# Kernel optimization log

Hardware: AMD Instinct MI355X
Metric: run time of the kernel (lower is better)

The kernel has to match this reference:

```python
import jax, jax.numpy as jnp
import numpy as np

D = 768
NH = 12
HD = D // NH
T = 8
HW = 14
B = 16
BT = B * T
NTOK = 1 + HW * HW  # 197
DH = int(D * 0.25)  # adapter hidden = 192
SCALE = 0.5


def _ln(x, g, b, eps=1e-5):
    # fp32 LayerNorm (matches LayerNorm subclass casting to fp32)
    xf = x.astype(jnp.float32)
    m = xf.mean(-1, keepdims=True)
    v = ((xf - m) ** 2).mean(-1, keepdims=True)
    return (((xf - m) / jnp.sqrt(v + eps)) * g + b).astype(x.dtype)


def _adapter(x, w1, b1, w2, b2, skip):
    h = jax.nn.gelu(x @ w1.T + b1, approximate=False)
    h = h @ w2.T + b2
    return x + h if skip else h


def _attention(xq, ykv, in_w, in_b, out_w, out_b):
    # xq: [Tx, N, D], ykv: [Ty, N, D]
    q = xq @ in_w[:D].T + in_b[:D]
    k = ykv @ in_w[D:2 * D].T + in_b[D:2 * D]
    v = ykv @ in_w[2 * D:].T + in_b[2 * D:]
    Tx, N, _ = q.shape
    Ty = k.shape[0]
    q = q.reshape(Tx, N, NH, HD).transpose(1, 2, 0, 3)  # [N,h,Tx,hd]
    k = k.reshape(Ty, N, NH, HD).transpose(1, 2, 0, 3)
    v = v.reshape(Ty, N, NH, HD).transpose(1, 2, 0, 3)
    aff = jnp.einsum('nhqd,nhkd->nhqk', q, k) / jnp.asarray(np.sqrt(HD), q.dtype)
    aff = jax.nn.softmax(aff, axis=-1)
    out = jnp.einsum('nhqk,nhkd->nhqd', aff, v)
    out = out.transpose(2, 0, 1, 3).reshape(Tx, N, D)
    return out @ out_w.T + out_b


_SHIFTS = (((0, 0), -4), ((0, 1), 1), ((1, 0), -1), ((0, 2), 2),
           ((2, 0), -2), ((1, 2), 3), ((2, 1), -3), ((2, 2), 4))


def _patch_shift(x):
    # x: [B, T, H, W, C]; roll along time on strided spatial grids
    out = x
    for (i, j), s in _SHIFTS:
        out = out.at[:, :, i::3, j::3, :].set(jnp.roll(x[:, :, i::3, j::3, :], s, axis=1))
    return out


def _forward(x, in_w, in_b, out_w, out_b, ln1_g, ln1_b, ln2_g, ln2_b,
             fc_w, fc_b, proj_w, proj_b,
             t1_w, t1_b, t2_w, t2_b,
             s1_w, s1_b, s2_w, s2_b,
             m1_w, m1_b, m2_w, m2_b):
    n, bt, d = x.shape
    b = bt // T
    # temporal attention on class token
    cls = x[:1]  # [1, bt, d]
    xt = cls.reshape(1, b, T, d).transpose(2, 1, 0, 3).reshape(T, b, d)
    xtn = _ln(xt, ln1_g, ln1_b)
    xt = _attention(xtn, xtn, in_w, in_b, out_w, out_b)
    xt = _adapter(xt, t1_w, t1_b, t2_w, t2_b, skip=False)
    xt = xt.reshape(T, b, 1, d).transpose(2, 1, 0, 3).reshape(1, bt, d)
    x = jnp.concatenate([x[:1], xt, x[1:]], axis=0)  # [n+1, bt, d]
    # spatial attention with patch shift (extra shifted K/V tokens)
    xln = _ln(x, ln1_g, ln1_b)
    tmp = xln[2:]  # [HW*HW, bt, d]
    tmp = tmp.reshape(HW, HW, b, T, d).transpose(2, 3, 0, 1, 4)  # b t h w c
    tmp = _patch_shift(tmp)
    tmp = tmp.transpose(2, 3, 0, 1, 4).reshape(HW * HW, bt, d)
    kv = jnp.concatenate([xln, tmp], axis=0)  # [2n+... , bt, d]
    attn_out = _attention(xln, kv, in_w, in_b, out_w, out_b)
    x = x + _adapter(attn_out, s1_w, s1_b, s2_w, s2_b, skip=True)
    # drop temporal token
    x = jnp.concatenate([x[:1], x[2:]], axis=0)
    # MLP + scaled MLP adapter
    xn = _ln(x, ln2_g, ln2_b)
    h = xn @ fc_w.T + fc_b
    h = h * jax.nn.sigmoid(1.702 * h)  # QuickGELU
    mlp = h @ proj_w.T + proj_b
    x = x + mlp + SCALE * _adapter(xn, m1_w, m1_b, m2_w, m2_b, skip=False)
    return x


def setup_inputs() -> dict:
    key = jax.random.key(0)
    ks = jax.random.split(key, 16)
    s = 0.02
    inp = {
        'x': jax.random.normal(ks[0], (NTOK, BT, D), jnp.float32),
        'in_w': jax.random.normal(ks[1], (3 * D, D), jnp.float32) * s,
        'in_b': jnp.zeros((3 * D,), jnp.float32),
        'out_w': jax.random.normal(ks[2], (D, D), jnp.float32) * s,
        'out_b': jnp.zeros((D,), jnp.float32),
        'ln1_g': jnp.ones((D,), jnp.float32),
        'ln1_b': jnp.zeros((D,), jnp.float32),
        'ln2_g': jnp.ones((D,), jnp.float32),
        'ln2_b': jnp.zeros((D,), jnp.float32),
        'fc_w': jax.random.normal(ks[3], (4 * D, D), jnp.float32) * s,
        'fc_b': jnp.zeros((4 * D,), jnp.float32),
        'proj_w': jax.random.normal(ks[4], (D, 4 * D), jnp.float32) * s,
        'proj_b': jnp.zeros((D,), jnp.float32),
        't1_w': jax.random.normal(ks[5], (DH, D), jnp.float32) * s,
        't1_b': jnp.zeros((DH,), jnp.float32),
        't2_w': jax.random.normal(ks[6], (D, DH), jnp.float32) * s,
        't2_b': jnp.zeros((D,), jnp.float32),
        's1_w': jax.random.normal(ks[7], (DH, D), jnp.float32) * s,
        's1_b': jnp.zeros((DH,), jnp.float32),
        's2_w': jax.random.normal(ks[8], (D, DH), jnp.float32) * s,
        's2_b': jnp.zeros((D,), jnp.float32),
        'm1_w': jax.random.normal(ks[9], (DH, D), jnp.float32) * s,
        'm1_b': jnp.zeros((DH,), jnp.float32),
        'm2_w': jax.random.normal(ks[10], (D, DH), jnp.float32) * s,
        'm2_b': jnp.zeros((D,), jnp.float32),
    }
    return inp


def reference(x, in_w, in_b, out_w, out_b, ln1_g, ln1_b, ln2_g, ln2_b,
              fc_w, fc_b, proj_w, proj_b,
              t1_w, t1_b, t2_w, t2_b,
              s1_w, s1_b, s2_w, s2_b,
              m1_w, m1_b, m2_w, m2_b):
    return _forward(x, in_w, in_b, out_w, out_b, ln1_g, ln1_b, ln2_g, ln2_b,
                    fc_w, fc_b, proj_w, proj_b,
                    t1_w, t1_b, t2_w, t2_b,
                    s1_w, s1_b, s2_w, s2_b,
                    m1_w, m1_b, m2_w, m2_b)
```

## Files before the change

kernel.cpp:

```cpp
#include <hip/hip_runtime.h>
#include <hip/hip_bf16.h>


#define DEV static __device__ __forceinline__

constexpr int D     = 768;
constexpr int TT    = 8;
constexpr int BT    = 128;
constexpr int NTOK  = 197;
constexpr int NTOK2 = 198;
constexpr int NKV   = 394;
constexpr int NKVP  = 448;
constexpr int NQP   = 224;
constexpr int NSZ   = 64;
constexpr int MQ    = NTOK2 * NSZ;
constexpr int MKV   = NKV   * NSZ;
constexpr int KCAT  = 3264;

constexpr int R2 = NTOK2 * BT;
constexpr int R3 = NTOK  * BT;

constexpr size_t O_WB  = 0;
constexpr size_t O_XLN = 3981312;
constexpr size_t O_AO  = O_XLN + 9732096;
constexpr size_t O_QT  = O_AO  + 9732096;
constexpr size_t O_KT  = O_QT  + 5505024;
constexpr size_t O_VT  = O_KT  + 11010048;
constexpr size_t O_SM  = O_VT  + 11010048;
constexpr size_t O_XT   = O_SM;
constexpr size_t O_XTN  = O_XT  + 98304;
constexpr size_t O_QKVT = O_XTN + 49152;
constexpr size_t O_AT   = O_QKVT+ 294912;
constexpr size_t O_ATP  = O_AT  + 49152;
constexpr size_t O_TH   = O_ATP + 49152;
constexpr size_t O_XT2  = O_TH  + 12288;
constexpr size_t O_MQ   = O_XT2 + 98304;
constexpr size_t O_MKV  = O_MQ  + 12672;
constexpr size_t O_CB   = O_MKV + 25216;

constexpr size_t WB_INW = 0;
constexpr size_t WB_OUTW= 1769472;
constexpr size_t WB_FCW = 2359296;
constexpr size_t WB_T1W = 7077888;
constexpr size_t WB_T2W = 7225344;
constexpr size_t WB_S1W = 7372800;
constexpr size_t WB_S2W = 7520256;
constexpr size_t WB_M1W = 7667712;

typedef __attribute__((ext_vector_type(8))) short bf16x8;
typedef __attribute__((ext_vector_type(4))) float f32x4;
#define MFMA16 __builtin_amdgcn_mfma_f32_16x16x32_bf16

DEV float bf2f(unsigned short u) { return __uint_as_float(((unsigned)u) << 16); }
DEV unsigned short f2bf(float f) {
    unsigned u = __float_as_uint(f);
    u += 0x7fffu + ((u >> 16) & 1u);
    return (unsigned short)(u >> 16);
}

DEV void gll16(const unsigned short* g, unsigned short* l) {
    __builtin_amdgcn_global_load_lds(
        (const __attribute__((address_space(1))) void*)g,
        (__attribute__((address_space(3))) void*)l, 16, 0, 0);
}

__global__ __launch_bounds__(256) void convert_k(const float* __restrict__ src,
                                                 unsigned short* __restrict__ dst, int n)
{
    int i = blockIdx.x * 256 + threadIdx.x;
    if (i < n) dst[i] = f2bf(src[i]);
}

__global__ __launch_bounds__(256) void convert2d_k(const float* __restrict__ src,
    int rows, int cols, int sld, unsigned short* __restrict__ dst, int dld, float scale)
{
    int i = blockIdx.x * 256 + threadIdx.x;
    if (i >= rows * cols) return;
    int r = i / cols, c = i % cols;
    dst[(size_t)r * dld + c] = f2bf(src[(size_t)r * sld + c] * scale);
}

__global__ __launch_bounds__(256) void combine_bias_k(const float* __restrict__ a,
    const float* __restrict__ b, float* __restrict__ cb)
{
    int i = blockIdx.x * 256 + threadIdx.x;
    if (i < 768) cb[i] = a[i] + 0.5f * b[i];
}

template<int EPI, int OMODE>
__global__ __launch_bounds__(256) void gemm_mfma_k(
    const unsigned short* __restrict__ A, const int* __restrict__ rowmap,
    const unsigned short* __restrict__ Wb, int wlda,
    const float* __restrict__ bias, float bscale,
    float* __restrict__ Yf, unsigned short* __restrict__ Yb,
    int N, int K, int ldy, const float* __restrict__ Xf)
{
    __shared__ unsigned short Als[128][32];
    __shared__ unsigned short Wls[64][32];
    const int tid = threadIdx.x;
    const int n0 = blockIdx.x * 64, m0 = blockIdx.y * 128;
    const int w = tid >> 6, l = tid & 63;

    int ga0 = m0 + w * 32 + (l >> 2);
    int ga1 = ga0 + 16;
    const int gw = n0 + w * 16 + (l >> 2);
    if (rowmap) { ga0 = rowmap[ga0]; ga1 = rowmap[ga1]; }
    const unsigned short* Ap0 = A + (size_t)ga0 * K + (l & 3) * 8;
    const unsigned short* Ap1 = A + (size_t)ga1 * K + (l & 3) * 8;
    const unsigned short* Wp  = Wb + (size_t)gw * wlda + (l & 3) * 8;
    unsigned short* lA0 = &Als[w * 32 + (l >> 2)][(l & 3) * 8];
    unsigned short* lA1 = &Als[w * 32 + 16 + (l >> 2)][(l & 3) * 8];
    unsigned short* lW  = &Wls[w * 16 + (l >> 2)][(l & 3) * 8];

    f32x4 acc[2][4];
    #pragma unroll
    for (int r = 0; r < 2; ++r)
        #pragma unroll
        for (int c = 0; c < 4; ++c)
            acc[r][c] = (f32x4){0.f, 0.f, 0.f, 0.f};

    for (int k0 = 0; k0 < K; k0 += 32) {
        __syncthreads();
        gll16(Ap0 + k0, lA0);
        gll16(Ap1 + k0, lA1);
        gll16(Wp  + k0, lW);
        __syncthreads();

        bf16x8 af[2], bfr[4];
        #pragma unroll
        for (int r = 0; r < 2; ++r)
            af[r] = *(const bf16x8*)&Als[w * 32 + r * 16 + (l & 15)][(l >> 4) * 8];
        #pragma unroll
        for (int c = 0; c < 4; ++c)
            bfr[c] = *(const bf16x8*)&Wls[c * 16 + (l & 15)][(l >> 4) * 8];
        #pragma unroll
        for (int r = 0; r < 2; ++r)
            #pragma unroll
            for (int c = 0; c < 4; ++c)
                acc[r][c] = MFMA16(af[r], bfr[c], acc[r][c], 0, 0, 0);
    }

    #pragma unroll
    for (int r = 0; r < 2; ++r) {
        #pragma unroll
        for (int c = 0; c < 4; ++c) {
            const int colg = n0 + c * 16 + (l & 15);
            const float bv = bscale * bias[colg];
            #pragma unroll
            for (int i = 0; i < 4; ++i) {
                const int rowg = m0 + w * 32 + r * 16 + ((l >> 4) << 2) + i;
                float v = acc[r][c][i] + bv;
                if (EPI == 1) v = 0.5f * v * (1.f + erff(v * 0.70710678118654752f));
                else if (EPI == 2) v = v / (1.f + __expf(-1.702f * v));
                if (OMODE == 0) {
                    Yf[(size_t)rowg * ldy + colg] = v;
                } else if (OMODE == 1) {
                    Yb[(size_t)rowg * ldy + colg] = f2bf(v);
                } else if (OMODE == 3) {
                    int j = rowg >> 6, bbl = rowg & 63, h = colg >> 6, d = colg & 63;
                    Yb[(((size_t)bbl * 12 + h) * NKVP + j) * 64 + d] = f2bf(v);
                } else if (OMODE == 5) {
                    int j = rowg >> 6, bbl = rowg & 63, h = colg >> 6, d = colg & 63;
                    Yb[(((size_t)bbl * 12 + h) * NQP + j) * 64 + d] = f2bf(v * 0.125f);
                } else if (OMODE == 6) {
                    Yf[(size_t)rowg * ldy + colg] += v;
                } else if (OMODE == 8) {
                    int tok2 = rowg >> 7, bb2 = rowg & 127;
                    if (tok2 != 1) {
                        int otok = tok2 ? tok2 - 1 : 0;
                        size_t oi = ((size_t)(otok * BT + bb2)) * ldy + colg;
                        Yf[oi] = Xf[oi] + bf2f(Yb[(size_t)rowg * ldy + colg]) + v;
                    }
                }
            }
        }
    }
}

template<typename TO>
__global__ __launch_bounds__(256) void ln_k(
    const float* __restrict__ in, TO* __restrict__ out,
    const float* __restrict__ g, const float* __restrict__ b, int rows)
{
    int w = (int)((blockIdx.x * 256 + threadIdx.x) >> 6);
    int lane = threadIdx.x & 63;
    if (w >= rows) return;
    const float* x = in + (size_t)w * D;
    float v[12];
    float s = 0.f;
    #pragma unroll
    for (int i = 0; i < 12; ++i) { v[i] = x[lane + 64 * i]; s += v[i]; }
    #pragma unroll
    for (int m = 32; m; m >>= 1) s += __shfl_xor(s, m);
    float mean = s * (1.f / 768.f);
    float s2 = 0.f;
    #pragma unroll
    for (int i = 0; i < 12; ++i) { float d0 = v[i] - mean; s2 += d0 * d0; }
    #pragma unroll
    for (int m = 32; m; m >>= 1) s2 += __shfl_xor(s2, m);
    float rstd = rsqrtf(s2 * (1.f / 768.f) + 1e-5f);
    TO* o = out + (size_t)w * D;
    #pragma unroll
    for (int i = 0; i < 12; ++i) {
        int c = lane + 64 * i;
        float y = (v[i] - mean) * rstd * g[c] + b[c];
        if constexpr (sizeof(TO) == 2) o[c] = f2bf(y); else o[c] = y;
    }
}

__global__ __launch_bounds__(256) void ln_gather_k(
    const float* __restrict__ x, const float* __restrict__ xt2,
    unsigned short* __restrict__ out,
    const float* __restrict__ g, const float* __restrict__ b)
{
    int w = (int)((blockIdx.x * 256 + threadIdx.x) >> 6);
    int lane = threadIdx.x & 63;
    if (w >= R2) return;
    int tok = w >> 7, bb = w & 127;
    const float* src;
    if (tok == 0)      src = x + (size_t)bb * D;
    else if (tok == 1) src = xt2 + (size_t)((bb & 7) * 16 + (bb >> 3)) * D;
    else               src = x + ((size_t)(tok - 1) * BT + bb) * D;
    float v[12];
    float s = 0.f;
    #pragma unroll
    for (int i = 0; i < 12; ++i) { v[i] = src[lane + 64 * i]; s += v[i]; }
    #pragma unroll
    for (int m = 32; m; m >>= 1) s += __shfl_xor(s, m);
    float mean = s * (1.f / 768.f);
    float s2 = 0.f;
    #pragma unroll
    for (int i = 0; i < 12; ++i) { float d0 = v[i] - mean; s2 += d0 * d0; }
    #pragma unroll
    for (int m = 32; m; m >>= 1) s2 += __shfl_xor(s2, m);
    float rstd = rsqrtf(s2 * (1.f / 768.f) + 1e-5f);
    unsigned short* o = out + (size_t)w * D;
    #pragma unroll
    for (int i = 0; i < 12; ++i) {
        int c = lane + 64 * i;
        o[c] = f2bf((v[i] - mean) * rstd * g[c] + b[c]);
    }
}

__global__ __launch_bounds__(256) void gather_cls_k(const float* __restrict__ x, float* __restrict__ xt)
{
    int idx = blockIdx.x * 256 + threadIdx.x;
    if (idx >= 128 * 768) return;
    int row = idx / 768, c = idx % 768;
    int t = row >> 4, bsel = row & 15;
    xt[idx] = x[(size_t)(bsel * TT + t) * D + c];
}

__global__ __launch_bounds__(64) void attn_temporal_k(
    const float* __restrict__ QKVt, unsigned short* __restrict__ Ot)
{
    int n = blockIdx.x, h = blockIdx.y;
    int lane = threadIdx.x;
    __shared__ float qs[8][64], ks[8][64], vs[8][64];
    __shared__ float ps[8][9];
    {
        int t = lane >> 3, f8 = lane & 7;
        size_t rb = ((size_t)(t * 16 + n)) * 2304 + h * 64 + f8 * 8;
        *(float4*)&qs[t][f8 * 8]     = *(const float4*)&QKVt[rb];
        *(float4*)&qs[t][f8 * 8 + 4] = *(const float4*)&QKVt[rb + 4];
        *(float4*)&ks[t][f8 * 8]     = *(const float4*)&QKVt[rb + 768];
        *(float4*)&ks[t][f8 * 8 + 4] = *(const float4*)&QKVt[rb + 772];
        *(float4*)&vs[t][f8 * 8]     = *(const float4*)&QKVt[rb + 1536];
        *(float4*)&vs[t][f8 * 8 + 4] = *(const float4*)&QKVt[rb + 1540];
    }
    __syncthreads();
    int qt = lane >> 3, kt = lane & 7;
    float s = 0.f;
    #pragma unroll
    for (int d0 = 0; d0 < 64; ++d0) s += qs[qt][d0] * ks[kt][d0];
    s *= 0.125f;
    float mx = s;
    #pragma unroll
    for (int m = 4; m; m >>= 1) mx = fmaxf(mx, __shfl_xor(mx, m));
    float p = __expf(s - mx), sum = p;
    #pragma unroll
    for (int m = 4; m; m >>= 1) sum += __shfl_xor(sum, m);
    ps[qt][kt] = p / sum;
    __syncthreads();
    int dg = lane & 7;
    float o[8] = {};
    #pragma unroll
    for (int k2 = 0; k2 < 8; ++k2) {
        float pp = ps[qt][k2];
        #pragma unroll
        for (int dd = 0; dd < 8; ++dd) o[dd] += pp * vs[k2][dg * 8 + dd];
    }
    unsigned short* op = &Ot[((size_t)(qt * 16 + n)) * D + h * 64 + dg * 8];
    #pragma unroll
    for (int dd = 0; dd < 8; ++dd) op[dd] = f2bf(o[dd]);
}

__global__ __launch_bounds__(256) void build_maps_k(int* __restrict__ mq,
                                                    int* __restrict__ mkv, int nbase)
{
    int idx = blockIdx.x * 256 + threadIdx.x;
    if (idx < MQ) {
        int j = idx >> 6, bbl = idx & 63;
        mq[idx] = j * BT + nbase + bbl;
    }
    int k = idx - MQ;
    if (k >= 0 && k < MKV) {
        int j = k >> 6, bb = nbase + (k & 63);
        int src;
        if (j < NTOK2) src = j * BT + bb;
        else {
            const int stab[9] = {-4, 1, 2, -1, 0, 3, -2, -3, 4};
            int p = j - NTOK2, r = p / 14, c = p % 14;
            int s = stab[(r % 3) * 3 + (c % 3)];
            int b = bb >> 3, t = bb & 7;
            int t2 = (t - s) & 7;
            src = (2 + p) * BT + b * TT + t2;
        }
        mkv[k] = src;
    }
}

__global__ __launch_bounds__(256) void attn_mfma_k(
    const unsigned short* __restrict__ Qt, const unsigned short* __restrict__ Kt,
    const unsigned short* __restrict__ Vt, unsigned short* __restrict__ AO, int nbase)
{
    const int qt0 = blockIdx.x * 32;
    const int h = blockIdx.y, nloc = blockIdx.z;
    const int tid = threadIdx.x, w = tid >> 6, l = tid & 63;
    __shared__ float Sls[32][68];
    __shared__ unsigned short Pls[32][72];
    __shared__ unsigned short Vls[64][72];
    __shared__ float mrun[32], lrun[32], alphals[32];

    const size_t baseQ = ((size_t)(nloc * 12 + h)) * NQP * 64;
    const size_t baseK = ((size_t)(nloc * 12 + h)) * NKVP * 64;

    bf16x8 qf[2][2];
    #pragma unroll
    for (int qb = 0; qb < 2; ++qb)
        #pragma unroll
        for (int ds = 0; ds < 2; ++ds)
            qf[qb][ds] = *(const bf16x8*)&Qt[baseQ + (size_t)(qt0 + qb * 16 + (l & 15)) * 64 + ds * 32 + (l >> 4) * 8];

    if (tid < 32) { mrun[tid] = -3e30f; lrun[tid] = 0.f; }
    f32x4 of[2];
    of[0] = (f32x4){0.f, 0.f, 0.f, 0.f};
    of[1] = (f32x4){0.f, 0.f, 0.f, 0.f};
    __syncthreads();

    for (int kv0 = 0; kv0 < NKV; kv0 += 64) {
        #pragma unroll
        for (int p = 0; p < 2; ++p) {
            int idx = tid + p * 256;
            int j = idx >> 3, seg = idx & 7;
            uint4 vv = *(const uint4*)&Vt[baseK + (size_t)(kv0 + j) * 64 + seg * 8];
            const unsigned short* pv = (const unsigned short*)&vv;
            #pragma unroll
            for (int e = 0; e < 8; ++e) Vls[seg * 8 + e][j] = pv[e];
        }
        f32x4 sa[2];
        sa[0] = (f32x4){0.f, 0.f, 0.f, 0.f};
        sa[1] = (f32x4){0.f, 0.f, 0.f, 0.f};
        #pragma unroll
        for (int ds = 0; ds < 2; ++ds) {
            bf16x8 kf = *(const bf16x8*)&Kt[baseK + (size_t)(kv0 + w * 16 + (l & 15)) * 64 + ds * 32 + (l >> 4) * 8];
            #pragma unroll
            for (int qb = 0; qb < 2; ++qb)
                sa[qb] = MFMA16(qf[qb][ds], kf, sa[qb], 0, 0, 0);
        }
        #pragma unroll
        for (int qb = 0; qb < 2; ++qb)
            #pragma unroll
            for (int i = 0; i < 4; ++i)
                Sls[qb * 16 + ((l >> 4) << 2) + i][w * 16 + (l & 15)] = sa[qb][i];
        __syncthreads();

        {
            int row = tid >> 3, cg = tid & 7;
            float sv[8], pv[8];
            float mx = -3e30f;
            #pragma unroll
            for (int j = 0; j < 8; ++j) {
                int c = cg * 8 + j;
                float s = (kv0 + c < NKV) ? Sls[row][c] : -3e30f;
                sv[j] = s; mx = fmaxf(mx, s);
            }
            mx = fmaxf(mx, __shfl_xor(mx, 1));
            mx = fmaxf(mx, __shfl_xor(mx, 2));
            mx = fmaxf(mx, __shfl_xor(mx, 4));
            float mold = mrun[row];
            float mnew = fmaxf(mold, mx);
            float ps = 0.f;
            #pragma unroll
            for (int j = 0; j < 8; ++j) { float p = __expf(sv[j] - mnew); pv[j] = p; ps += p; }
            ps += __shfl_xor(ps, 1);
            ps += __shfl_xor(ps, 2);
            ps += __shfl_xor(ps, 4);
            if (cg == 0) {
                float al = __expf(mold - mnew);
                alphals[row] = al;
                mrun[row] = mnew;
                lrun[row] = lrun[row] * al + ps;
            }
            #pragma unroll
            for (int j = 0; j < 8; ++j) Pls[row][cg * 8 + j] = f2bf(pv[j]);
        }
        __syncthreads();

        #pragma unroll
        for (int qb = 0; qb < 2; ++qb) {
            #pragma unroll
            for (int i = 0; i < 4; ++i)
                of[qb][i] *= alphals[qb * 16 + ((l >> 4) << 2) + i];
        }
        #pragma unroll
        for (int ks = 0; ks < 2; ++ks) {
            bf16x8 vf = *(const bf16x8*)&Vls[w * 16 + (l & 15)][ks * 32 + (l >> 4) * 8];
            #pragma unroll
            for (int qb = 0; qb < 2; ++qb) {
                bf16x8 pf = *(const bf16x8*)&Pls[qb * 16 + (l & 15)][ks * 32 + (l >> 4) * 8];
                of[qb] = MFMA16(pf, vf, of[qb], 0, 0, 0);
            }
        }
        __syncthreads();
    }

    #pragma unroll
    for (int qb = 0; qb < 2; ++qb) {
        #pragma unroll
        for (int i = 0; i < 4; ++i) {
            int qrow = qb * 16 + ((l >> 4) << 2) + i;
            int q = qt0 + qrow;
            if (q < NTOK2) {
                float inv = 1.f / lrun[qrow];
                AO[((size_t)q * BT + nbase + nloc) * D + h * 64 + w * 16 + (l & 15)] = f2bf(of[qb][i] * inv);
            }
        }
    }
}

extern "C" void kernel_launch(void* const* d_in, const int* in_sizes, int n_in,
                              void* d_out, int out_size, void* d_ws, size_t ws_size,
                              hipStream_t stream)
{
    const float* x    = (const float*)d_in[0];
    const float* in_w = (const float*)d_in[1];
    const float* in_b = (const float*)d_in[2];
    const float* outw = (const float*)d_in[3];
    const float* outb = (const float*)d_in[4];
    const float* ln1g = (const float*)d_in[5];
    const float* ln1b = (const float*)d_in[6];
    const float* ln2g = (const float*)d_in[7];
    const float* ln2b = (const float*)d_in[8];
    const float* fcw  = (const float*)d_in[9];
    const float* fcb  = (const float*)d_in[10];
    const float* pjw  = (const float*)d_in[11];
    const float* pjb  = (const float*)d_in[12];
    const float* t1w  = (const float*)d_in[13];
    const float* t1b  = (const float*)d_in[14];
    const float* t2w  = (const float*)d_in[15];
    const float* t2b  = (const float*)d_in[16];
    const float* s1w  = (const float*)d_in[17];
    const float* s1b  = (const float*)d_in[18];
    const float* s2w  = (const float*)d_in[19];
    const float* s2b  = (const float*)d_in[20];
    const float* m1w  = (const float*)d_in[21];
    const float* m1b  = (const float*)d_in[22];
    const float* m2w  = (const float*)d_in[23];
    const float* m2b  = (const float*)d_in[24];

    float* ws  = (float*)d_ws;
    float* out = (float*)d_out;

    unsigned short* WB = (unsigned short*)(ws + O_WB);
    unsigned short* w_in  = WB + WB_INW;
    unsigned short* w_out = WB + WB_OUTW;
    unsigned short* w_fc  = WB + WB_FCW;
    unsigned short* w_t1  = WB + WB_T1W;
    unsigned short* w_t2  = WB + WB_T2W;
    unsigned short* w_s1  = WB + WB_S1W;
    unsigned short* w_s2  = WB + WB_S2W;
    unsigned short* w_m1  = WB + WB_M1W;

    unsigned short* xln  = (unsigned short*)(ws + O_XLN);
    unsigned short* AO   = (unsigned short*)(ws + O_AO);
    unsigned short* Qt   = (unsigned short*)(ws + O_QT);
    unsigned short* Kt   = (unsigned short*)(ws + O_KT);
    unsigned short* Vt   = (unsigned short*)(ws + O_VT);
    unsigned short* ao2b = xln;
    unsigned short* xn   = AO;
    unsigned short* h192 = Qt;
    unsigned short* pjcat= (unsigned short*)(ws + O_QT + 2433024);
    unsigned short* catb = Kt;

    float* xt            = ws + O_XT;
    unsigned short* xtn  = (unsigned short*)(ws + O_XTN);
    float* qkvt          = ws + O_QKVT;
    unsigned short* at   = (unsigned short*)(ws + O_AT);
    unsigned short* atp  = (unsigned short*)(ws + O_ATP);
    unsigned short* th   = (unsigned short*)(ws + O_TH);
    float* xt2           = ws + O_XT2;
    int*   mapq          = (int*)(ws + O_MQ);
    int*   mapkv         = (int*)(ws + O_MKV);
    float* cb            = ws + O_CB;

    auto conv = [&](const float* s, unsigned short* dst, int n) {
        convert_k<<<(n + 255) / 256, 256, 0, stream>>>(s, dst, n);
    };
    conv(in_w, w_in, 2304 * 768);
    conv(outw, w_out, 768 * 768);
    conv(fcw,  w_fc,  3072 * 768);
    conv(t1w,  w_t1,  192 * 768);
    conv(t2w,  w_t2,  768 * 192);
    conv(s1w,  w_s1,  192 * 768);
    conv(s2w,  w_s2,  768 * 192);
    conv(m1w,  w_m1,  192 * 768);
    combine_bias_k<<<3, 256, 0, stream>>>(pjb, m2b, cb);

    gather_cls_k<<<384, 256, 0, stream>>>(x, xt);
    ln_k<unsigned short><<<32, 256, 0, stream>>>(xt, xtn, ln1g, ln1b, 128);
    gemm_mfma_k<0,0><<<dim3(36,1), 256, 0, stream>>>(xtn, nullptr, w_in, 768, in_b, 1.f, qkvt, nullptr, 2304, 768, 2304, nullptr);
    attn_temporal_k<<<dim3(16,12), 64, 0, stream>>>(qkvt, at);
    gemm_mfma_k<0,1><<<dim3(12,1), 256, 0, stream>>>(at,  nullptr, w_out, 768, outb, 1.f, nullptr, atp, 768, 768, 768, nullptr);
    gemm_mfma_k<1,1><<<dim3(3,1),  256, 0, stream>>>(atp, nullptr, w_t1,  768, t1b, 1.f, nullptr, th,  192, 768, 192, nullptr);
    gemm_mfma_k<0,0><<<dim3(12,1), 256, 0, stream>>>(th,  nullptr, w_t2,  192, t2b, 1.f, xt2, nullptr, 768, 192, 768, nullptr);

    ln_gather_k<<<6336, 256, 0, stream>>>(x, xt2, xln, ln1g, ln1b);

    for (int c = 0; c < 2; ++c) {
        const int nbase = c * NSZ;
        build_maps_k<<<148, 256, 0, stream>>>(mapq, mapkv, nbase);
        gemm_mfma_k<0,5><<<dim3(12,99),  256, 0, stream>>>(xln, mapq,  w_in,              768, in_b,        1.f, nullptr, Qt, 768, 768, 768, nullptr);
        gemm_mfma_k<0,3><<<dim3(12,197), 256, 0, stream>>>(xln, mapkv, w_in + 768 * 768,  768, in_b + 768,  1.f, nullptr, Kt, 768, 768, 768, nullptr);
        gemm_mfma_k<0,3><<<dim3(12,197), 256, 0, stream>>>(xln, mapkv, w_in + 1536 * 768, 768, in_b + 1536, 1.f, nullptr, Vt, 768, 768, 768, nullptr);
        attn_mfma_k<<<dim3(7,12,64), 256, 0, stream>>>(Qt, Kt, Vt, AO, nbase);
    }

    convert2d_k<<<9216, 256, 0, stream>>>(pjw, 768, 3072, 3072, pjcat, KCAT, 1.f);
    convert2d_k<<<576,  256, 0, stream>>>(m2w, 768, 192, 192, pjcat + 3072, KCAT, 0.5f);

    gemm_mfma_k<0,1><<<dim3(12,198), 256, 0, stream>>>(AO,   nullptr, w_out, 768, outb, 1.f, nullptr, ao2b, 768, 768, 768, nullptr);
    gemm_mfma_k<1,1><<<dim3(3,198),  256, 0, stream>>>(ao2b, nullptr, w_s1,  768, s1b,  1.f, nullptr, h192, 192, 768, 192, nullptr);
    gemm_mfma_k<0,8><<<dim3(12,198), 256, 0, stream>>>(h192, nullptr, w_s2,  192, s2b,  1.f, out, ao2b, 768, 192, 768, x);

    ln_k<unsigned short><<<6304, 256, 0, stream>>>(out, xn, ln2g, ln2b, R3);
    const int nbm[4] = {49, 49, 49, 50};
    int moff = 0;
    for (int mc = 0; mc < 4; ++mc) {
        const int nb = nbm[mc];
        gemm_mfma_k<2,1><<<dim3(48,nb), 256, 0, stream>>>(xn + (size_t)moff * 768, nullptr, w_fc, 768, fcb, 1.f, nullptr, catb, 3072, 768, KCAT, nullptr);
        gemm_mfma_k<1,1><<<dim3(3,nb),  256, 0, stream>>>(xn + (size_t)moff * 768, nullptr, w_m1, 768, m1b, 1.f, nullptr, catb + 3072, 192, 768, KCAT, nullptr);
        gemm_mfma_k<0,6><<<dim3(12,nb), 256, 0, stream>>>(catb, nullptr, pjcat, KCAT, cb, 1.f, out + (size_t)moff * 768, nullptr, 768, KCAT, 768, nullptr);
        moff += nb * 128;
    }
}
```

Baseline: 1.670 ms.

## Add 128x128 MFMA GEMM tile and loop attention over query tiles per block

Adds a 128x128-tile GEMM kernel (each wave computes a 64x64 sub-tile) and uses it for every GEMM whose N is a multiple of 128. The 64-wide kernel is kept for the N=192 adapter layers. The goal is higher arithmetic intensity and fewer redundant A-tile loads. The attention kernel now loops over all query tiles inside one block per (head, batch), instead of one block per query tile. This cuts block count and may improve K/V cache reuse, but it lowers parallelism and reloads K/V per query tile serially.

```diff
diff --git a/kernel.cpp b/kernel.cpp
--- a/kernel.cpp
+++ b/kernel.cpp
@@ -88,12 +88,111 @@
 }
 
 template<int EPI, int OMODE>
-__global__ __launch_bounds__(256) void gemm_mfma_k(
+DEV void epi_store(float v0, int rowg, int colg, const float* bias, float bscale,
+                   float* Yf, unsigned short* Yb, int ldy, const float* Xf)
+{
+    float v = v0 + bscale * bias[colg];
+    if (EPI == 1) v = 0.5f * v * (1.f + erff(v * 0.70710678118654752f));
+    else if (EPI == 2) v = v / (1.f + __expf(-1.702f * v));
+    if (OMODE == 0) {
+        Yf[(size_t)rowg * ldy + colg] = v;
+    } else if (OMODE == 1) {
+        Yb[(size_t)rowg * ldy + colg] = f2bf(v);
+    } else if (OMODE == 3) {
+        int j = rowg >> 6, bbl = rowg & 63, h = colg >> 6, d = colg & 63;
+        Yb[(((size_t)bbl * 12 + h) * NKVP + j) * 64 + d] = f2bf(v);
+    } else if (OMODE == 5) {
+        int j = rowg >> 6, bbl = rowg & 63, h = colg >> 6, d = colg & 63;
+        Yb[(((size_t)bbl * 12 + h) * NQP + j) * 64 + d] = f2bf(v * 0.125f);
+    } else if (OMODE == 6) {
+        Yf[(size_t)rowg * ldy + colg] += v;
+    } else if (OMODE == 8) {
+        int tok2 = rowg >> 7, bb2 = rowg & 127;
+        if (tok2 != 1) {
+            int otok = tok2 ? tok2 - 1 : 0;
+            size_t oi = ((size_t)(otok * BT + bb2)) * ldy + colg;
+            Yf[oi] = Xf[oi] + bf2f(Yb[(size_t)rowg * ldy + colg]) + v;
+        }
+    }
+}
+
+template<int EPI, int OMODE>
+__global__ __launch_bounds__(256) void gemm128_k(
     const unsigned short* __restrict__ A, const int* __restrict__ rowmap,
     const unsigned short* __restrict__ Wb, int wlda,
     const float* __restrict__ bias, float bscale,
     float* __restrict__ Yf, unsigned short* __restrict__ Yb,
-    int N, int K, int ldy, const float* __restrict__ Xf)
+    int ldy, int K, const float* __restrict__ Xf)
+{
+    __shared__ unsigned short Als[128][32];
+    __shared__ unsigned short Bls[128][32];
+    const int tid = threadIdx.x;
+    const int n0 = blockIdx.x * 128, m0 = blockIdx.y * 128;
+    const int w = tid >> 6, l = tid & 63;
+    const int wr = w >> 1, wc = w & 1;
+
+    const int srow = tid >> 2, sch = (tid & 3) * 8;
+    int ga0 = m0 + srow, ga1 = m0 + 64 + srow;
+    if (rowmap) { ga0 = rowmap[ga0]; ga1 = rowmap[ga1]; }
+    const unsigned short* Ap0 = A + (size_t)ga0 * K + sch;
+    const unsigned short* Ap1 = A + (size_t)ga1 * K + sch;
+    const unsigned short* Wp0 = Wb + (size_t)(n0 + srow) * wlda + sch;
+    const unsigned short* Wp1 = Wb + (size_t)(n0 + 64 + srow) * wlda + sch;
+    unsigned short* lA0 = &Als[srow][sch];
+    unsigned short* lA1 = &Als[64 + srow][sch];
+    unsigned short* lB0 = &Bls[srow][sch];
+    unsigned short* lB1 = &Bls[64 + srow][sch];
+
+    f32x4 acc[4][4];
+    #pragma unroll
+    for (int r = 0; r < 4; ++r)
+        #pragma unroll
+        for (int c = 0; c < 4; ++c)
+            acc[r][c] = (f32x4){0.f, 0.f, 0.f, 0.f};
+
+    for (int k0 = 0; k0 < K; k0 += 32) {
+        __syncthreads();
+        gll16(Ap0 + k0, lA0);
+        gll16(Ap1 + k0, lA1);
+        gll16(Wp0 + k0, lB0);
+        gll16(Wp1 + k0, lB1);
+        __syncthreads();
+
+        bf16x8 af[4], bfr[4];
+        #pragma unroll
+        for (int r = 0; r < 4; ++r)
+            af[r] = *(const bf16x8*)&Als[wr * 64 + r * 16 + (l & 15)][(l >> 4) * 8];
+        #pragma unroll
+        for (int c = 0; c < 4; ++c)
+            bfr[c] = *(const bf16x8*)&Bls[wc * 64 + c * 16 + (l & 15)][(l >> 4) * 8];
+        #pragma unroll
+        for (int r = 0; r < 4; ++r)
+            #pragma unroll
+            for (int c = 0; c < 4; ++c)
+                acc[r][c] = MFMA16(af[r], bfr[c], acc[r][c], 0, 0, 0);
+    }
+
+    #pragma unroll
+    for (int r = 0; r < 4; ++r) {
+        #pragma unroll
+        for (int c = 0; c < 4; ++c) {
+            const int colg = n0 + wc * 64 + c * 16 + (l & 15);
+            #pragma unroll
+            for (int i = 0; i < 4; ++i) {
+                const int rowg = m0 + wr * 64 + r * 16 + ((l >> 4) << 2) + i;
+                epi_store<EPI, OMODE>(acc[r][c][i], rowg, colg, bias, bscale, Yf, Yb, ldy, Xf);
+            }
+        }
+    }
+}
+
+template<int EPI, int OMODE>
+__global__ __launch_bounds__(256) void gemm64_k(
+    const unsigned short* __restrict__ A, const int* __restrict__ rowmap,
+    const unsigned short* __restrict__ Wb, int wlda,
+    const float* __restrict__ bias, float bscale,
+    float* __restrict__ Yf, unsigned short* __restrict__ Yb,
+    int ldy, int K, const float* __restrict__ Xf)
 {
     __shared__ unsigned short Als[128][32];
     __shared__ unsigned short Wls[64][32];
@@ -145,33 +244,10 @@
         #pragma unroll
         for (int c = 0; c < 4; ++c) {
             const int colg = n0 + c * 16 + (l & 15);
-            const float bv = bscale * bias[colg];
             #pragma unroll
             for (int i = 0; i < 4; ++i) {
                 const int rowg = m0 + w * 32 + r * 16 + ((l >> 4) << 2) + i;
-                float v = acc[r][c][i] + bv;
-                if (EPI == 1) v = 0.5f * v * (1.f + erff(v * 0.70710678118654752f));
-                else if (EPI == 2) v = v / (1.f + __expf(-1.702f * v));
-                if (OMODE == 0) {
-                    Yf[(size_t)rowg * ldy + colg] = v;
-                } else if (OMODE == 1) {
-                    Yb[(size_t)rowg * ldy + colg] = f2bf(v);
-                } else if (OMODE == 3) {
-                    int j = rowg >> 6, bbl = rowg & 63, h = colg >> 6, d = colg & 63;
-                    Yb[(((size_t)bbl * 12 + h) * NKVP + j) * 64 + d] = f2bf(v);
-                } else if (OMODE == 5) {
-                    int j = rowg >> 6, bbl = rowg & 63, h = colg >> 6, d = colg & 63;
-                    Yb[(((size_t)bbl * 12 + h) * NQP + j) * 64 + d] = f2bf(v * 0.125f);
-                } else if (OMODE == 6) {
-                    Yf[(size_t)rowg * ldy + colg] += v;
-                } else if (OMODE == 8) {
-                    int tok2 = rowg >> 7, bb2 = rowg & 127;
-                    if (tok2 != 1) {
-                        int otok = tok2 ? tok2 - 1 : 0;
-                        size_t oi = ((size_t)(otok * BT + bb2)) * ldy + colg;
-                        Yf[oi] = Xf[oi] + bf2f(Yb[(size_t)rowg * ldy + colg]) + v;
-                    }
-                }
+                epi_store<EPI, OMODE>(acc[r][c][i], rowg, colg, bias, bscale, Yf, Yb, ldy, Xf);
             }
         }
     }
@@ -324,8 +400,7 @@
     const unsigned short* __restrict__ Qt, const unsigned short* __restrict__ Kt,
     const unsigned short* __restrict__ Vt, unsigned short* __restrict__ AO, int nbase)
 {
-    const int qt0 = blockIdx.x * 32;
-    const int h = blockIdx.y, nloc = blockIdx.z;
+    const int h = blockIdx.x, nloc = blockIdx.y;
     const int tid = threadIdx.x, w = tid >> 6, l = tid & 63;
     __shared__ float Sls[32][68];
     __shared__ unsigned short Pls[32][72];
@@ -335,105 +410,109 @@
     const size_t baseQ = ((size_t)(nloc * 12 + h)) * NQP * 64;
     const size_t baseK = ((size_t)(nloc * 12 + h)) * NKVP * 64;
 
-    bf16x8 qf[2][2];
-    #pragma unroll
-    for (int qb = 0; qb < 2; ++qb)
-        #pragma unroll
-        for (int ds = 0; ds < 2; ++ds)
-            qf[qb][ds] = *(const bf16x8*)&Qt[baseQ + (size_t)(qt0 + qb * 16 + (l & 15)) * 64 + ds * 32 + (l >> 4) * 8];
-
-    if (tid < 32) { mrun[tid] = -3e30f; lrun[tid] = 0.f; }
-    f32x4 of[2];
-    of[0] = (f32x4){0.f, 0.f, 0.f, 0.f};
-    of[1] = (f32x4){0.f, 0.f, 0.f, 0.f};
-    __syncthreads();
-
-    for (int kv0 = 0; kv0 < NKV; kv0 += 64) {
-        #pragma unroll
-        for (int p = 0; p < 2; ++p) {
-            int idx = tid + p * 256;
-            int j = idx >> 3, seg = idx & 7;
-            uint4 vv = *(const uint4*)&Vt[baseK + (size_t)(kv0 + j) * 64 + seg * 8];
-            const unsigned short* pv = (const unsigned short*)&vv;
-            #pragma unroll
-            for (int e = 0; e < 8; ++e) Vls[seg * 8 + e][j] = pv[e];
+    for (int qt0 = 0; qt0 < NTOK2; qt0 += 32) {
+        __syncthreads();
+        if (tid < 32) { mrun[tid] = -3e30f; lrun[tid] = 0.f; }
+
+        bf16x8 qf[2][2];
+        #pragma unroll
+        for (int qb = 0; qb < 2; ++qb)
+            #pragma unroll
+            for (int ds = 0; ds < 2; ++ds)
+                qf[qb][ds] = *(const bf16x8*)&Qt[baseQ + (size_t)(qt0 + qb * 16 + (l & 15)) * 64 + ds * 32 + (l >> 4) * 8];
+
+        f32x4 of[2];
+        of[0] = (f32x4){0.f, 0.f, 0.f, 0.f};
+        of[1] = (f32x4){0.f, 0.f, 0.f, 0.f};
+        __syncthreads();
+
+        for (int kv0 = 0; kv0 < NKV; kv0 += 64) {
+            #pragma unroll
+            for (int p = 0; p < 2; ++p) {
+                int idx = tid + p * 256;
+                int j = idx >> 3, seg = idx & 7;
+                uint4 vv = *(const uint4*)&Vt[baseK + (size_t)(kv0 + j) * 64 + seg * 8];
+                const unsigned short* pv = (const unsigned short*)&vv;
+                #pragma unroll
+                for (int e = 0; e < 8; ++e) Vls[seg * 8 + e][j] = pv[e];
+            }
+            f32x4 sa[2];
+            sa[0] = (f32x4){0.f, 0.f, 0.f, 0.f};
+            sa[1] = (f32x4){0.f, 0.f, 0.f, 0.f};
+            #pragma unroll
+            for (int ds = 0; ds < 2; ++ds) {
+                bf16x8 kf = *(const bf16x8*)&Kt[baseK + (size_t)(kv0 + w * 16 + (l & 15)) * 64 + ds * 32 + (l >> 4) * 8];
+                #pragma unroll
+                for (int qb = 0; qb < 2; ++qb)
+                    sa[qb] = MFMA16(qf[qb][ds], kf, sa[qb], 0, 0, 0);
+            }
+            #pragma unroll
+            for (int qb = 0; qb < 2; ++qb)
+                #pragma unroll
+                for (int i = 0; i < 4; ++i)
+                    Sls[qb * 16 + ((l >> 4) << 2) + i][w * 16 + (l & 15)] = sa[qb][i];
+            __syncthreads();
+
+            {
+                int row = tid >> 3, cg = tid & 7;
+                float sv[8], pv[8];
+                float mx = -3e30f;
+                #pragma unroll
+                for (int j = 0; j < 8; ++j) {
+                    int c = cg * 8 + j;
+                    float s = (kv0 + c < NKV) ? Sls[row][c] : -3e30f;
+                    sv[j] = s; mx = fmaxf(mx, s);
+                }
+                mx = fmaxf(mx, __shfl_xor(mx, 1));
+                mx = fmaxf(mx, __shfl_xor(mx, 2));
+                mx = fmaxf(mx, __shfl_xor(mx, 4));
+                float mold = mrun[row];
+                float mnew = fmaxf(mold, mx);
+                float ps = 0.f;
+                #pragma unroll
+                for (int j = 0; j < 8; ++j) { float p = __expf(sv[j] - mnew); pv[j] = p; ps += p; }
+                ps += __shfl_xor(ps, 1);
+                ps += __shfl_xor(ps, 2);
+                ps += __shfl_xor(ps, 4);
+                if (cg == 0) {
+                    float al = __expf(mold - mnew);
+                    alphals[row] = al;
+                    mrun[row] = mnew;
+                    lrun[row] = lrun[row] * al + ps;
+                }
+                #pragma unroll
+                for (int j = 0; j < 8; ++j) Pls[row][cg * 8 + j] = f2bf(pv[j]);
+            }
+            __syncthreads();
+
+            #pragma unroll
+            for (int qb = 0; qb < 2; ++qb) {
+                #pragma unroll
+                for (int i = 0; i < 4; ++i)
+                    of[qb][i] *= alphals[qb * 16 + ((l >> 4) << 2) + i];
+            }
+            #pragma unroll
+            for (int ks = 0; ks < 2; ++ks) {
+                bf16x8 vf = *(const bf16x8*)&Vls[w * 16 + (l & 15)][ks * 32 + (l >> 4) * 8];
+                #pragma unroll
+                for (int qb = 0; qb < 2; ++qb) {
+                    bf16x8 pf = *(const bf16x8*)&Pls[qb * 16 + (l & 15)][ks * 32 + (l >> 4) * 8];
+                    of[qb] = MFMA16(pf, vf, of[qb], 0, 0, 0);
+                }
+            }
+            __syncthreads();
         }
-        f32x4 sa[2];
-        sa[0] = (f32x4){0.f, 0.f, 0.f, 0.f};
-        sa[1] = (f32x4){0.f, 0.f, 0.f, 0.f};
-        #pragma unroll
-        for (int ds = 0; ds < 2; ++ds) {
-            bf16x8 kf = *(const bf16x8*)&Kt[baseK + (size_t)(kv0 + w * 16 + (l & 15)) * 64 + ds * 32 + (l >> 4) * 8];
-            #pragma unroll
-            for (int qb = 0; qb < 2; ++qb)
-                sa[qb] = MFMA16(qf[qb][ds], kf, sa[qb], 0, 0, 0);
-        }
-        #pragma unroll
-        for (int qb = 0; qb < 2; ++qb)
-            #pragma unroll
-            for (int i = 0; i < 4; ++i)
-                Sls[qb * 16 + ((l >> 4) << 2) + i][w * 16 + (l & 15)] = sa[qb][i];
-        __syncthreads();
-
-        {
-            int row = tid >> 3, cg = tid & 7;
-            float sv[8], pv[8];
-            float mx = -3e30f;
-            #pragma unroll
-            for (int j = 0; j < 8; ++j) {
-                int c = cg * 8 + j;
-                float s = (kv0 + c < NKV) ? Sls[row][c] : -3e30f;
-                sv[j] = s; mx = fmaxf(mx, s);
-            }
-            mx = fmaxf(mx, __shfl_xor(mx, 1));
-            mx = fmaxf(mx, __shfl_xor(mx, 2));
-            mx = fmaxf(mx, __shfl_xor(mx, 4));
-            float mold = mrun[row];
-            float mnew = fmaxf(mold, mx);
-            float ps = 0.f;
-            #pragma unroll
-            for (int j = 0; j < 8; ++j) { float p = __expf(sv[j] - mnew); pv[j] = p; ps += p; }
-            ps += __shfl_xor(ps, 1);
-            ps += __shfl_xor(ps, 2);
-            ps += __shfl_xor(ps, 4);
-            if (cg == 0) {
-                float al = __expf(mold - mnew);
-                alphals[row] = al;
-                mrun[row] = mnew;
-                lrun[row] = lrun[row] * al + ps;
-            }
-            #pragma unroll
-            for (int j = 0; j < 8; ++j) Pls[row][cg * 8 + j] = f2bf(pv[j]);
-        }
-        __syncthreads();
 
         #pragma unroll
         for (int qb = 0; qb < 2; ++qb) {
             #pragma unroll
-            for (int i = 0; i < 4; ++i)
-                of[qb][i] *= alphals[qb * 16 + ((l >> 4) << 2) + i];
-        }
-        #pragma unroll
-        for (int ks = 0; ks < 2; ++ks) {
-            bf16x8 vf = *(const bf16x8*)&Vls[w * 16 + (l & 15)][ks * 32 + (l >> 4) * 8];
-            #pragma unroll
-            for (int qb = 0; qb < 2; ++qb) {
-                bf16x8 pf = *(const bf16x8*)&Pls[qb * 16 + (l & 15)][ks * 32 + (l >> 4) * 8];
-                of[qb] = MFMA16(pf, vf, of[qb], 0, 0, 0);
-            }
-        }
-        __syncthreads();
-    }
-
-    #pragma unroll
-    for (int qb = 0; qb < 2; ++qb) {
-        #pragma unroll
-        for (int i = 0; i < 4; ++i) {
-            int qrow = qb * 16 + ((l >> 4) << 2) + i;
-            int q = qt0 + qrow;
-            if (q < NTOK2) {
-                float inv = 1.f / lrun[qrow];
-                AO[((size_t)q * BT + nbase + nloc) * D + h * 64 + w * 16 + (l & 15)] = f2bf(of[qb][i] * inv);
+            for (int i = 0; i < 4; ++i) {
+                int qrow = qb * 16 + ((l >> 4) << 2) + i;
+                int q = qt0 + qrow;
+                if (q < NTOK2) {
+                    float inv = 1.f / lrun[qrow];
+                    AO[((size_t)q * BT + nbase + nloc) * D + h * 64 + w * 16 + (l & 15)] = f2bf(of[qb][i] * inv);
+                }
             }
         }
     }
@@ -519,38 +598,38 @@
 
     gather_cls_k<<<384, 256, 0, stream>>>(x, xt);
     ln_k<unsigned short><<<32, 256, 0, stream>>>(xt, xtn, ln1g, ln1b, 128);
-    gemm_mfma_k<0,0><<<dim3(36,1), 256, 0, stream>>>(xtn, nullptr, w_in, 768, in_b, 1.f, qkvt, nullptr, 2304, 768, 2304, nullptr);
+    gemm128_k<0,0><<<dim3(18,1), 256, 0, stream>>>(xtn, nullptr, w_in, 768, in_b, 1.f, qkvt, nullptr, 2304, 768, nullptr);
     attn_temporal_k<<<dim3(16,12), 64, 0, stream>>>(qkvt, at);
-    gemm_mfma_k<0,1><<<dim3(12,1), 256, 0, stream>>>(at,  nullptr, w_out, 768, outb, 1.f, nullptr, atp, 768, 768, 768, nullptr);
-    gemm_mfma_k<1,1><<<dim3(3,1),  256, 0, stream>>>(atp, nullptr, w_t1,  768, t1b, 1.f, nullptr, th,  192, 768, 192, nullptr);
-    gemm_mfma_k<0,0><<<dim3(12,1), 256, 0, stream>>>(th,  nullptr, w_t2,  192, t2b, 1.f, xt2, nullptr, 768, 192, 768, nullptr);
+    gemm128_k<0,1><<<dim3(6,1), 256, 0, stream>>>(at,  nullptr, w_out, 768, outb, 1.f, nullptr, atp, 768, 768, nullptr);
+    gemm64_k<1,1><<<dim3(3,1),  256, 0, stream>>>(atp, nullptr, w_t1,  768, t1b, 1.f, nullptr, th,  192, 768, nullptr);
+    gemm128_k<0,0><<<dim3(6,1), 256, 0, stream>>>(th,  nullptr, w_t2,  192, t2b, 1.f, xt2, nullptr, 768, 192, nullptr);
 
     ln_gather_k<<<6336, 256, 0, stream>>>(x, xt2, xln, ln1g, ln1b);
 
     for (int c = 0; c < 2; ++c) {
         const int nbase = c * NSZ;
         build_maps_k<<<148, 256, 0, stream>>>(mapq, mapkv, nbase);
-        gemm_mfma_k<0,5><<<dim3(12,99),  256, 0, stream>>>(xln, mapq,  w_in,              768, in_b,        1.f, nullptr, Qt, 768, 768, 768, nullptr);
-        gemm_mfma_k<0,3><<<dim3(12,197), 256, 0, stream>>>(xln, mapkv, w_in + 768 * 768,  768, in_b + 768,  1.f, nullptr, Kt, 768, 768, 768, nullptr);
-        gemm_mfma_k<0,3><<<dim3(12,197), 256, 0, stream>>>(xln, mapkv, w_in + 1536 * 768, 768, in_b + 1536, 1.f, nullptr, Vt, 768, 768, 768, nullptr);
-        attn_mfma_k<<<dim3(7,12,64), 256, 0, stream>>>(Qt, Kt, Vt, AO, nbase);
+        gemm128_k<0,5><<<dim3(6,99),  256, 0, stream>>>(xln, mapq,  w_in,              768, in_b,        1.f, nullptr, Qt, 768, 768, nullptr);
+        gemm128_k<0,3><<<dim3(6,197), 256, 0, stream>>>(xln, mapkv, w_in + 768 * 768,  768, in_b + 768,  1.f, nullptr, Kt, 768, 768, nullptr);
+        gemm128_k<0,3><<<dim3(6,197), 256, 0, stream>>>(xln, mapkv, w_in + 1536 * 768, 768, in_b + 1536, 1.f, nullptr, Vt, 768, 768, nullptr);
+        attn_mfma_k<<<dim3(12,64), 256, 0, stream>>>(Qt, Kt, Vt, AO, nbase);
     }
 
     convert2d_k<<<9216, 256, 0, stream>>>(pjw, 768, 3072, 3072, pjcat, KCAT, 1.f);
     convert2d_k<<<576,  256, 0, stream>>>(m2w, 768, 192, 192, pjcat + 3072, KCAT, 0.5f);
 
-    gemm_mfma_k<0,1><<<dim3(12,198), 256, 0, stream>>>(AO,   nullptr, w_out, 768, outb, 1.f, nullptr, ao2b, 768, 768, 768, nullptr);
-    gemm_mfma_k<1,1><<<dim3(3,198),  256, 0, stream>>>(ao2b, nullptr, w_s1,  768, s1b,  1.f, nullptr, h192, 192, 768, 192, nullptr);
-    gemm_mfma_k<0,8><<<dim3(12,198), 256, 0, stream>>>(h192, nullptr, w_s2,  192, s2b,  1.f, out, ao2b, 768, 192, 768, x);
+    gemm128_k<0,1><<<dim3(6,198), 256, 0, stream>>>(AO,   nullptr, w_out, 768, outb, 1.f, nullptr, ao2b, 768, 768, nullptr);
+    gemm64_k<1,1><<<dim3(3,198),  256, 0, stream>>>(ao2b, nullptr, w_s1,  768, s1b,  1.f, nullptr, h192, 192, 768, nullptr);
+    gemm128_k<0,8><<<dim3(6,198), 256, 0, stream>>>(h192, nullptr, w_s2,  192, s2b,  1.f, out, ao2b, 768, 192, x);
 
     ln_k<unsigned short><<<6304, 256, 0, stream>>>(out, xn, ln2g, ln2b, R3);
     const int nbm[4] = {49, 49, 49, 50};
     int moff = 0;
     for (int mc = 0; mc < 4; ++mc) {
         const int nb = nbm[mc];
-        gemm_mfma_k<2,1><<<dim3(48,nb), 256, 0, stream>>>(xn + (size_t)moff * 768, nullptr, w_fc, 768, fcb, 1.f, nullptr, catb, 3072, 768, KCAT, nullptr);
-        gemm_mfma_k<1,1><<<dim3(3,nb),  256, 0, stream>>>(xn + (size_t)moff * 768, nullptr, w_m1, 768, m1b, 1.f, nullptr, catb + 3072, 192, 768, KCAT, nullptr);
-        gemm_mfma_k<0,6><<<dim3(12,nb), 256, 0, stream>>>(catb, nullptr, pjcat, KCAT, cb, 1.f, out + (size_t)moff * 768, nullptr, 768, KCAT, 768, nullptr);
+        gemm128_k<2,1><<<dim3(24,nb), 256, 0, stream>>>(xn + (size_t)moff * 768, nullptr, w_fc, 768, fcb, 1.f, nullptr, catb, KCAT, 768, nullptr);
+        gemm64_k<1,1><<<dim3(3,nb),  256, 0, stream>>>(xn + (size_t)moff * 768, nullptr, w_m1, 768, m1b, 1.f, nullptr, catb + 3072, KCAT, 768, nullptr);
+        gemm128_k<0,6><<<dim3(6,nb), 256, 0, stream>>>(catb, nullptr, pjcat, KCAT, cb, 1.f, out + (size_t)moff * 768, nullptr, 768, KCAT, nullptr);
         moff += nb * 128;
     }
 }
```

Result: slower. 1.791 ms (+7.2%).
